# Kernel optimization log

Measured on AMD Instinct MI355X. Metric: run time of the kernel, lower is better.

The kernel has to match this reference:

```python
import jax, jax.numpy as jnp
import numpy as np

B, S, H = 2, 2048, 2048
NQ, NKV, DH = 16, 8, 128
EPS = 1e-6
ROPE_BASE = 10000.0


def setup_inputs() -> dict:
    key = jax.random.key(0)
    ks = jax.random.split(key, 6)
    hidden_states = jax.random.normal(ks[0], (B, S, H), dtype=jnp.float32)
    # real RoPE tables
    inv_freq = 1.0 / (ROPE_BASE ** (jnp.arange(0, DH, 2, dtype=jnp.float32) / DH))
    pos = jnp.arange(S, dtype=jnp.float32)
    freqs = pos[:, None] * inv_freq[None, :]              # [S, DH/2]
    emb = jnp.concatenate([freqs, freqs], axis=-1)        # [S, DH]
    cos = jnp.broadcast_to(jnp.cos(emb)[None], (B, S, DH))
    sin = jnp.broadcast_to(jnp.sin(emb)[None], (B, S, DH))
    # additive causal mask [1,1,S,S]
    causal = jnp.tril(jnp.ones((S, S), dtype=bool))
    attention_mask = jnp.where(causal, 0.0, jnp.finfo(jnp.float32).min)[None, None]
    q_w = jax.random.normal(ks[1], (H, H), dtype=jnp.float32) * 0.02
    k_w = jax.random.normal(ks[2], (NKV * DH, H), dtype=jnp.float32) * 0.02
    v_w = jax.random.normal(ks[3], (NKV * DH, H), dtype=jnp.float32) * 0.02
    o_w = jax.random.normal(ks[4], (H, H), dtype=jnp.float32) * 0.02
    return {"hidden_states": hidden_states, "cos": cos, "sin": sin,
            "attention_mask": attention_mask,
            "q_w": q_w, "k_w": k_w, "v_w": v_w, "o_w": o_w}


def _rotate_half(x):
    x1, x2 = jnp.split(x, 2, axis=-1)
    return jnp.concatenate([-x2, x1], axis=-1)


def _l2norm(x, eps=EPS):
    # weightless RMS norm over head_dim (Llama4TextL2Norm)
    return x * jax.lax.rsqrt(jnp.mean(x * x, axis=-1, keepdims=True) + eps)


def reference(hidden_states, cos, sin, attention_mask, q_w, k_w, v_w, o_w):
    b, s, _ = hidden_states.shape
    # projections (no bias) -> [B, n_heads, S, DH]
    q = jnp.einsum('bsh,dh->bsd', hidden_states, q_w).reshape(b, s, NQ, DH).transpose(0, 2, 1, 3)
    k = jnp.einsum('bsh,dh->bsd', hidden_states, k_w).reshape(b, s, NKV, DH).transpose(0, 2, 1, 3)
    v = jnp.einsum('bsh,dh->bsd', hidden_states, v_w).reshape(b, s, NKV, DH).transpose(0, 2, 1, 3)
    # NanoChat negates sin before standard HF rotary
    sin_e = (-sin)[:, None, :, :]   # [B,1,S,DH]
    cos_e = cos[:, None, :, :]
    q = q * cos_e + _rotate_half(q) * sin_e
    k = k * cos_e + _rotate_half(k) * sin_e
    # weightless QK RMS norm
    q = _l2norm(q)
    k = _l2norm(k)
    # GQA: repeat kv heads
    groups = NQ // NKV
    k = jnp.repeat(k, groups, axis=1)
    v = jnp.repeat(v, groups, axis=1)
    scaling = DH ** -0.5
    scores = jnp.einsum('bhqd,bhkd->bhqk', q, k) * scaling + attention_mask
    probs = jax.nn.softmax(scores, axis=-1)
    attn = jnp.einsum('bhqk,bhkd->bhqd', probs, v)           # [B,H,S,DH]
    attn = attn.transpose(0, 2, 1, 3).reshape(b, s, NQ * DH)
    out = jnp.einsum('bsd,hd->bsh', attn, o_w)
    return out
```

## Files before the change

kernel.cpp:

```cpp
#include <hip/hip_runtime.h>

typedef unsigned short ushort_t;
typedef __bf16 bf16x8 __attribute__((ext_vector_type(8)));
typedef float f32x4 __attribute__((ext_vector_type(4)));
typedef unsigned int u32x4 __attribute__((ext_vector_type(4)));
typedef unsigned short us4 __attribute__((ext_vector_type(4)));
typedef unsigned short us8 __attribute__((ext_vector_type(8)));

#define DEVINL __device__ __forceinline__

DEVINL ushort_t f2bf(float f) {
    unsigned u = __float_as_uint(f);
    u += 0x7FFF + ((u >> 16) & 1);
    return (ushort_t)(u >> 16);
}
DEVINL float bf2f(ushort_t h) { return __uint_as_float(((unsigned)h) << 16); }

DEVINL void gload_lds16(const void* g, void* l) {
    __builtin_amdgcn_global_load_lds(
        (const __attribute__((address_space(1))) void*)g,
        (__attribute__((address_space(3))) void*)l, 16, 0, 0);
}

DEVINL bf16x8 ld_frag(const ushort_t* p) {
    us8 v = *(const us8*)p;
    return __builtin_bit_cast(bf16x8, v);
}

__global__ __launch_bounds__(256) void convert_all(const f32x4* __restrict__ h,
                                                   const f32x4* __restrict__ qw,
                                                   const f32x4* __restrict__ kw,
                                                   const f32x4* __restrict__ vw,
                                                   const f32x4* __restrict__ ow,
                                                   us4* __restrict__ hb,
                                                   us4* __restrict__ wqkv,
                                                   us4* __restrict__ owb) {
    const int N0 = 2097152;
    const int N1 = 1048576;
    const int N2 = 524288;
    const int N3 = 524288;
    int i = blockIdx.x * 256 + threadIdx.x;
    const f32x4* src; us4* dst;
    if (i < N0)                               { src = h  + i;                 dst = hb + i; }
    else if ((i -= N0) < N1)                  { src = qw + i;                 dst = wqkv + i; }
    else if ((i -= N1) < N2)                  { src = kw + i;                 dst = wqkv + 1048576 + i; }
    else if ((i -= N2) < N3)                  { src = vw + i;                 dst = wqkv + 1572864 + i; }
    else                                      { i -= N3; src = ow + i;       dst = owb + i; }
    f32x4 f = *src;
    us4 o;
    o[0] = f2bf(f[0]); o[1] = f2bf(f[1]); o[2] = f2bf(f[2]); o[3] = f2bf(f[3]);
    *dst = o;
}

template <typename OutT>
__global__ __launch_bounds__(256) void gemm_bt(const ushort_t* __restrict__ A,
                                               const ushort_t* __restrict__ W,
                                               OutT* __restrict__ C,
                                               int M, int N, int K) {
    __shared__ ushort_t As[2][128 * 32];
    __shared__ ushort_t Bs[2][128 * 32];
    const int t = threadIdx.x;
    const int w = t >> 6, lane = t & 63;
    const int quad = lane >> 4, l16 = lane & 15;
    const int sw = (l16 >> 1) & 3;
    const int lid = blockIdx.x;
    const int xcd = lid & 7, j = lid >> 3;
    const int r = j & 15, st = j >> 4;
    const int bm = (xcd * 4 + (r & 3)) * 128;
    const int bn = (st * 4 + (r >> 2)) * 128;
    const int wr = (w >> 1) * 64, wc = (w & 1) * 64;

    f32x4 acc[4][4];
#pragma unroll
    for (int i = 0; i < 4; i++)
#pragma unroll
        for (int jj = 0; jj < 4; jj++) acc[i][jj] = f32x4{0.f, 0.f, 0.f, 0.f};

    auto stage = [&](int k0, int buf) {
#pragma unroll
        for (int i = 0; i < 2; i++) {
            int u = i * 256 + t;
            int row = u >> 2;
            int ce = ((u & 3) ^ ((row >> 1) & 3)) * 8;
            gload_lds16(A + (size_t)(bm + row) * K + k0 + ce, (char*)As[buf] + u * 16);
            gload_lds16(W + (size_t)(bn + row) * K + k0 + ce, (char*)Bs[buf] + u * 16);
        }
    };

    stage(0, 0);
    int sbuf = 0;
    for (int k0 = 0; k0 < K; k0 += 32) {
        __syncthreads();
        const int nb = sbuf ^ 1;
        if (k0 + 32 < K) stage(k0 + 32, nb);
        const ushort_t* Ab = As[sbuf];
        const ushort_t* Bb = Bs[sbuf];
        sbuf = nb;
        bf16x8 af[4], bf[4];
#pragma unroll
        for (int mt = 0; mt < 4; mt++)
            af[mt] = ld_frag(&Ab[(wr + mt * 16 + l16) * 32 + (quad ^ sw) * 8]);
#pragma unroll
        for (int nt = 0; nt < 4; nt++)
            bf[nt] = ld_frag(&Bb[(wc + nt * 16 + l16) * 32 + (quad ^ sw) * 8]);
#pragma unroll
        for (int mt = 0; mt < 4; mt++)
#pragma unroll
            for (int nt = 0; nt < 4; nt++)
                acc[mt][nt] = __builtin_amdgcn_mfma_f32_16x16x32_bf16(af[mt], bf[nt],
                                                                      acc[mt][nt], 0, 0, 0);
    }

#pragma unroll
    for (int mt = 0; mt < 4; mt++)
#pragma unroll
        for (int nt = 0; nt < 4; nt++) {
            int row = bm + wr + mt * 16 + quad * 4;
            int col = bn + wc + nt * 16 + l16;
#pragma unroll
            for (int rr = 0; rr < 4; rr++) {
                float v = acc[mt][nt][rr];
                if constexpr (sizeof(OutT) == 2)
                    C[(size_t)(row + rr) * N + col] = (OutT)f2bf(v);
                else
                    C[(size_t)(row + rr) * N + col] = v;
            }
        }
}

__global__ __launch_bounds__(256) void rope_norm(const ushort_t* __restrict__ qkv,
                                                 const float* __restrict__ cosb,
                                                 const float* __restrict__ sinb,
                                                 ushort_t* __restrict__ q,
                                                 ushort_t* __restrict__ k) {
    int row = blockIdx.x;
    int b = row >> 11, s = row & 2047;
    int w = threadIdx.x >> 6, lane = threadIdx.x & 63;
    int hh = blockIdx.y * 4 + w;
    const ushort_t* src = qkv + (size_t)row * 4096 + hh * 128;
    float x1 = bf2f(src[lane]);
    float x2 = bf2f(src[lane + 64]);
    float c = cosb[(size_t)row * 128 + lane];
    float sn = sinb[(size_t)row * 128 + lane];
    float y1 = x1 * c + x2 * sn;
    float y2 = x2 * c - x1 * sn;
    float ss = y1 * y1 + y2 * y2;
#pragma unroll
    for (int off = 1; off < 64; off <<= 1) ss += __shfl_xor(ss, off);
    float rinv = rsqrtf(ss * (1.0f / 128.0f) + 1e-6f);
    y1 *= rinv; y2 *= rinv;
    ushort_t* dst;
    if (hh < 16) dst = q + (((size_t)(b * 16 + hh)) * 2048 + s) * 128;
    else         dst = k + (((size_t)(b * 8 + hh - 16)) * 2048 + s) * 128;
    dst[lane] = f2bf(y1);
    dst[lane + 64] = f2bf(y2);
}

__global__ __launch_bounds__(256) void v_transpose(const ushort_t* __restrict__ qkv,
                                                   ushort_t* __restrict__ vt) {
    __shared__ ushort_t tile[64 * 72];
    int t = threadIdx.x;
    int s0 = blockIdx.x * 64, d0 = blockIdx.y * 64, bh = blockIdx.z;
    int b = bh >> 3, kvh = bh & 7;
    {
        int sl = t >> 2, c = t & 3;
        const ushort_t* src = qkv + (size_t)(b * 2048 + s0 + sl) * 4096 + 3072 + kvh * 128 + d0 + c * 16;
        u32x4 v0 = *(const u32x4*)src;
        u32x4 v1 = *(const u32x4*)(src + 8);
        *(u32x4*)&tile[sl * 72 + c * 16] = v0;
        *(u32x4*)&tile[sl * 72 + c * 16 + 8] = v1;
    }
    __syncthreads();
    {
        int dl = t >> 2, c = t & 3;
        alignas(16) ushort_t tmp[16];
#pragma unroll
        for (int i = 0; i < 16; i++) tmp[i] = tile[(c * 16 + i) * 72 + dl];
        ushort_t* dst = vt + (size_t)(bh * 128 + d0 + dl) * 2048 + s0 + c * 16;
        *(u32x4*)dst = *(const u32x4*)&tmp[0];
        *(u32x4*)(dst + 8) = *(const u32x4*)&tmp[8];
    }
}

__global__ __launch_bounds__(256) void flash_attn(const ushort_t* __restrict__ q,
                                                  const ushort_t* __restrict__ k,
                                                  const ushort_t* __restrict__ vt,
                                                  ushort_t* __restrict__ attn) {
    __shared__ ushort_t Ks[2][4 * 64 * 32];
    __shared__ ushort_t Vts[2][2 * 128 * 32];
    __shared__ ushort_t Ps[4 * 32 * 72];
    const int t = threadIdx.x;
    const int w = t >> 6, lane = t & 63;
    const int quad = lane >> 4, l16 = lane & 15;
    const int sw = (l16 >> 1) & 3;
    const int lid = blockIdx.x;
    const int xcd = lid & 7, jj = lid >> 3;
    const int g = xcd * 2 + (jj >> 4);
    const int p = jj & 15;
    const int b = g >> 3, kvh = g & 7;
    const int h0 = kvh * 2;
    const size_t kbase = ((size_t)(b * 8 + kvh)) * 2048 * 128;
    const size_t vbase = ((size_t)(b * 8 + kvh)) * 128 * 2048;

    const float C1 = 0.12751744f;
    const float C2 = 1.45f;

    auto stage = [&](int j0, int buf) {
#pragma unroll
        for (int i = 0; i < 4; i++) {
            int u = i * 256 + t;
            int qd = u >> 8, rr = (u >> 2) & 63;
            int c4 = ((u & 3) ^ ((rr >> 1) & 3)) * 8;
            gload_lds16(k + kbase + (size_t)(j0 + rr) * 128 + qd * 32 + c4,
                        (char*)Ks[buf] + u * 16);
        }
#pragma unroll
        for (int i = 0; i < 4; i++) {
            int u = i * 256 + t;
            int ks = u >> 9, dd = (u >> 2) & 127;
            int c4 = ((u & 3) ^ ((dd >> 1) & 3)) * 8;
            gload_lds16(vt + vbase + (size_t)dd * 2048 + j0 + ks * 32 + c4,
                        (char*)Vts[buf] + u * 16);
        }
    };

    const int qtile0 = 31 - p;
    stage(0, 0);
    int sbuf = 0;

    for (int pass = 0; pass < 2; ++pass) {
        const int qi = pass ? p : qtile0;
        const int q0 = qi * 64;

        bf16x8 qf[2][4];
#pragma unroll
        for (int h = 0; h < 2; h++) {
            const size_t qbase = ((size_t)(b * 16 + h0 + h) * 2048 + q0 + w * 16 + l16) * 128;
#pragma unroll
            for (int qd = 0; qd < 4; qd++) {
                us8 v = *(const us8*)(q + qbase + qd * 32 + quad * 8);
                qf[h][qd] = __builtin_bit_cast(bf16x8, v);
            }
        }

        f32x4 o[2][8];
#pragma unroll
        for (int h = 0; h < 2; h++)
#pragma unroll
            for (int i = 0; i < 8; i++) o[h][i] = f32x4{0.f, 0.f, 0.f, 0.f};
        float lsum[2][4];
#pragma unroll
        for (int h = 0; h < 2; h++)
#pragma unroll
            for (int r = 0; r < 4; r++) lsum[h][r] = 0.f;

        for (int jt = 0; jt <= qi; ++jt) {
            const int j0 = jt * 64;
            const bool diag = (jt == qi);
            __syncthreads();
            const int nb = sbuf ^ 1;
            if (jt < qi)            stage((jt + 1) * 64, nb);
            else if (pass == 0)     stage(0, nb);
            const ushort_t* Kb = Ks[sbuf];
            const ushort_t* Vb = Vts[sbuf];
            sbuf = nb;

            f32x4 sc[2][4];
#pragma unroll
            for (int h = 0; h < 2; h++)
#pragma unroll
                for (int c = 0; c < 4; c++) sc[h][c] = f32x4{0.f, 0.f, 0.f, 0.f};
#pragma unroll
            for (int c = 0; c < 4; c++)
#pragma unroll
                for (int qd = 0; qd < 4; qd++) {
                    bf16x8 kf = ld_frag(&Kb[qd * 2048 + (c * 16 + l16) * 32 + (quad ^ sw) * 8]);
                    sc[0][c] = __builtin_amdgcn_mfma_f32_16x16x32_bf16(qf[0][qd], kf, sc[0][c], 0, 0, 0);
                    sc[1][c] = __builtin_amdgcn_mfma_f32_16x16x32_bf16(qf[1][qd], kf, sc[1][c], 0, 0, 0);
                }

#pragma unroll
            for (int c = 0; c < 4; c++)
#pragma unroll
                for (int r = 0; r < 4; r++) {
                    float p0 = __builtin_amdgcn_exp2f(sc[0][c][r] * C1 - C2);
                    float p1 = __builtin_amdgcn_exp2f(sc[1][c][r] * C1 - C2);
                    if (diag) {
                        int kg = j0 + c * 16 + l16;
                        int qg = q0 + w * 16 + quad * 4 + r;
                        if (kg > qg) { p0 = 0.f; p1 = 0.f; }
                    }
                    lsum[0][r] += p0;
                    lsum[1][r] += p1;
                    Ps[w * 2304 + (quad * 4 + r) * 72 + c * 16 + l16] = f2bf(p0);
                    Ps[w * 2304 + (16 + quad * 4 + r) * 72 + c * 16 + l16] = f2bf(p1);
                }

#pragma unroll
            for (int ks = 0; ks < 2; ks++) {
                bf16x8 pf0 = ld_frag(&Ps[w * 2304 + l16 * 72 + ks * 32 + quad * 8]);
                bf16x8 pf1 = ld_frag(&Ps[w * 2304 + (16 + l16) * 72 + ks * 32 + quad * 8]);
#pragma unroll
                for (int od = 0; od < 8; od++) {
                    bf16x8 vf = ld_frag(&Vb[ks * 4096 + (od * 16 + l16) * 32 + (quad ^ sw) * 8]);
                    o[0][od] = __builtin_amdgcn_mfma_f32_16x16x32_bf16(pf0, vf, o[0][od], 0, 0, 0);
                    o[1][od] = __builtin_amdgcn_mfma_f32_16x16x32_bf16(pf1, vf, o[1][od], 0, 0, 0);
                }
            }
        }

        float rl[2][4];
#pragma unroll
        for (int h = 0; h < 2; h++)
#pragma unroll
            for (int r = 0; r < 4; r++) {
                float s = lsum[h][r];
#pragma unroll
                for (int off = 1; off < 16; off <<= 1) s += __shfl_xor(s, off);
                rl[h][r] = 1.0f / s;
            }
#pragma unroll
        for (int h = 0; h < 2; h++) {
            const size_t obase = ((size_t)(b * 2048 + q0 + w * 16 + quad * 4)) * 2048 + (h0 + h) * 128;
#pragma unroll
            for (int od = 0; od < 8; od++)
#pragma unroll
                for (int r = 0; r < 4; r++)
                    attn[obase + (size_t)r * 2048 + od * 16 + l16] = f2bf(o[h][od][r] * rl[h][r]);
        }
    }
}

extern "C" void kernel_launch(void* const* d_in, const int* in_sizes, int n_in,
                              void* d_out, int out_size, void* d_ws, size_t ws_size,
                              hipStream_t stream) {
    (void)in_sizes; (void)n_in; (void)out_size; (void)ws_size;
    const float* hidden = (const float*)d_in[0];
    const float* cosb   = (const float*)d_in[1];
    const float* sinb   = (const float*)d_in[2];
    const float* q_w    = (const float*)d_in[4];
    const float* k_w    = (const float*)d_in[5];
    const float* v_w    = (const float*)d_in[6];
    const float* o_w    = (const float*)d_in[7];

    char* ws = (char*)d_ws;
    ushort_t* hb   = (ushort_t*)(ws);
    ushort_t* wqkv = (ushort_t*)(ws + (16ull << 20));
    ushort_t* owb  = (ushort_t*)(ws + (32ull << 20));
    ushort_t* qkv  = (ushort_t*)(ws + (40ull << 20));
    ushort_t* attn = qkv;
    ushort_t* qb   = (ushort_t*)(ws + (72ull << 20));
    ushort_t* kb   = (ushort_t*)(ws + (88ull << 20));
    ushort_t* vt   = (ushort_t*)(ws + (96ull << 20));

    convert_all<<<20480, 256, 0, stream>>>((const f32x4*)hidden, (const f32x4*)q_w,
                                           (const f32x4*)k_w, (const f32x4*)v_w,
                                           (const f32x4*)o_w,
                                           (us4*)hb, (us4*)wqkv, (us4*)owb);

    gemm_bt<ushort_t><<<1024, 256, 0, stream>>>(hb, wqkv, qkv, 4096, 4096, 2048);
    rope_norm<<<dim3(4096, 6), 256, 0, stream>>>(qkv, cosb, sinb, qb, kb);
    v_transpose<<<dim3(32, 2, 16), 256, 0, stream>>>(qkv, vt);
    flash_attn<<<256, 256, 0, stream>>>(qb, kb, vt, attn);
    gemm_bt<float><<<512, 256, 0, stream>>>(attn, owb, (float*)d_out, 4096, 2048, 2048);
}
```

Baseline: 371.9 us.

## Triple-buffer LDS staging in GEMM and flash attention with partial vmcnt waits

```diff
diff --git a/kernel.cpp b/kernel.cpp
--- a/kernel.cpp
+++ b/kernel.cpp
@@ -26,6 +26,10 @@
     us8 v = *(const us8*)p;
     return __builtin_bit_cast(bf16x8, v);
 }
+
+#define BARRIER_KEEP4()  asm volatile("s_waitcnt vmcnt(4)\n\ts_barrier" ::: "memory")
+#define BARRIER_KEEP8()  asm volatile("s_waitcnt vmcnt(8)\n\ts_barrier" ::: "memory")
+#define BARRIER_KEEP0()  asm volatile("s_waitcnt vmcnt(0)\n\ts_barrier" ::: "memory")
 
 __global__ __launch_bounds__(256) void convert_all(const f32x4* __restrict__ h,
                                                    const f32x4* __restrict__ qw,
@@ -57,8 +61,8 @@
                                                const ushort_t* __restrict__ W,
                                                OutT* __restrict__ C,
                                                int M, int N, int K) {
-    __shared__ ushort_t As[2][128 * 32];
-    __shared__ ushort_t Bs[2][128 * 32];
+    __shared__ ushort_t As[3][128 * 32];
+    __shared__ ushort_t Bs[3][128 * 32];
     const int t = threadIdx.x;
     const int w = t >> 6, lane = t & 63;
     const int quad = lane >> 4, l16 = lane & 15;
@@ -87,15 +91,18 @@
         }
     };
 
+    const int NIT = K >> 5;
     stage(0, 0);
-    int sbuf = 0;
-    for (int k0 = 0; k0 < K; k0 += 32) {
-        __syncthreads();
-        const int nb = sbuf ^ 1;
-        if (k0 + 32 < K) stage(k0 + 32, nb);
-        const ushort_t* Ab = As[sbuf];
-        const ushort_t* Bb = Bs[sbuf];
-        sbuf = nb;
+    stage(32, 1);
+    int cb = 0, pb = 2;
+    for (int n = 0; n < NIT; ++n) {
+        if (n + 1 < NIT) BARRIER_KEEP4();
+        else             BARRIER_KEEP0();
+        if (n + 2 < NIT) stage((n + 2) * 32, pb);
+        const ushort_t* Ab = As[cb];
+        const ushort_t* Bb = Bs[cb];
+        cb = cb == 2 ? 0 : cb + 1;
+        pb = pb == 2 ? 0 : pb + 1;
         bf16x8 af[4], bf[4];
 #pragma unroll
         for (int mt = 0; mt < 4; mt++)
@@ -186,8 +193,8 @@
                                                   const ushort_t* __restrict__ k,
                                                   const ushort_t* __restrict__ vt,
                                                   ushort_t* __restrict__ attn) {
-    __shared__ ushort_t Ks[2][4 * 64 * 32];
-    __shared__ ushort_t Vts[2][2 * 128 * 32];
+    __shared__ ushort_t Ks[3][4 * 64 * 32];
+    __shared__ ushort_t Vts[3][2 * 128 * 32];
     __shared__ ushort_t Ps[4 * 32 * 72];
     const int t = threadIdx.x;
     const int w = t >> 6, lane = t & 63;
@@ -225,8 +232,12 @@
     };
 
     const int qtile0 = 31 - p;
-    stage(0, 0);
-    int sbuf = 0;
+    const int S_total = qtile0 + 1 + p + 1;
+    auto j0_of = [&](int s) { return (s <= qtile0 ? s : s - qtile0 - 1) * 64; };
+
+    stage(j0_of(0), 0);
+    stage(j0_of(1), 1);
+    int sidx = 0, cb = 0, pb = 2;
 
     for (int pass = 0; pass < 2; ++pass) {
         const int qi = pass ? p : qtile0;
@@ -257,13 +268,14 @@
         for (int jt = 0; jt <= qi; ++jt) {
             const int j0 = jt * 64;
             const bool diag = (jt == qi);
-            __syncthreads();
-            const int nb = sbuf ^ 1;
-            if (jt < qi)            stage((jt + 1) * 64, nb);
-            else if (pass == 0)     stage(0, nb);
-            const ushort_t* Kb = Ks[sbuf];
-            const ushort_t* Vb = Vts[sbuf];
-            sbuf = nb;
+            if (sidx + 1 < S_total) BARRIER_KEEP8();
+            else                    BARRIER_KEEP0();
+            if (sidx + 2 < S_total) stage(j0_of(sidx + 2), pb);
+            const ushort_t* Kb = Ks[cb];
+            const ushort_t* Vb = Vts[cb];
+            cb = cb == 2 ? 0 : cb + 1;
+            pb = pb == 2 ? 0 : pb + 1;
+            sidx++;
 
             f32x4 sc[2][4];
 #pragma unroll
```

New measurement: 370.5 us. About the same (-0.4%).
